# Kernel tuning notes

Measured on AMD Instinct MI355X. Metric: run time of the kernel, lower is better.

Reference implementation:

```python
import jax, jax.numpy as jnp
import numpy as np

IN_FEATURES = 4096
OUT_FEATURES = 4096
MAX_RANK = 32
ALPHA = 32
SCALING = ALPHA / MAX_RANK  # 1.0


def setup_inputs() -> dict:
    key = jax.random.key(0)
    k_x, k_u, k_v = jax.random.split(key, 3)
    x = jax.random.normal(k_x, (4, 2048, IN_FEATURES), dtype=jnp.float32)
    U = jax.random.normal(k_u, (OUT_FEATURES, MAX_RANK), dtype=jnp.float32) * 0.01
    S = jnp.ones((MAX_RANK,), dtype=jnp.float32)
    V = jax.random.normal(k_v, (MAX_RANK, IN_FEATURES), dtype=jnp.float32) * 0.01
    return {"x": x, "U": U, "S": S, "V": V}


def reference(x, U, S, V):
    # Original: W = U @ diag(S) @ V ; out = (x @ W.T) * scaling  (dropout=0 -> Identity)
    # Mathematically identical factored form: ((x @ V^T) * S) @ U^T * scaling.
    h = jnp.einsum('bsi,ri->bsr', x, V)        # [B,S,rank]
    h = h * S                                   # scale by singular values
    out = jnp.einsum('bsr,or->bso', h, U)       # [B,S,out]
    return out * SCALING
```

## Files before the change

### kernel.cpp

```cpp
#include <hip/hip_runtime.h>
#include <hip/hip_bf16.h>

typedef __bf16 bf16x8 __attribute__((ext_vector_type(8)));
typedef float  f32x4  __attribute__((ext_vector_type(4)));

#define IN_F   4096
#define OUT_F  4096
#define RANK   32

__device__ __forceinline__ bf16x8 cvt8(float4 a, float4 b) {
    bf16x8 r;
    r[0] = (__bf16)a.x; r[1] = (__bf16)a.y; r[2] = (__bf16)a.z; r[3] = (__bf16)a.w;
    r[4] = (__bf16)b.x; r[5] = (__bf16)b.y; r[6] = (__bf16)b.z; r[7] = (__bf16)b.w;
    return r;
}

template <int NSL>
__global__ __launch_bounds__(256, 3)
void lora_h(const float* __restrict__ X, const float* __restrict__ S,
            const float* __restrict__ V, float* __restrict__ Hpart)
{
    constexpr int SL    = IN_F / NSL;
    constexpr int STEPS = SL / 32;

    __shared__ float Hp[4][64][33];

    const int tid  = threadIdx.x;
    const int wave = tid >> 6;
    const int lane = tid & 63;
    const int r    = lane & 15;
    const int kg   = lane >> 4;

    const int t0 = blockIdx.x * 64;
    const int f0 = (blockIdx.y * 4 + wave) * SL;

    f32x4 acc[4][2] = {};

    const float* xb0 = X + (size_t)(t0 + r) * IN_F + f0 + kg * 8;
    const float* vb0 = V + (size_t)r * IN_F + f0 + kg * 8;

    #pragma unroll 2
    for (int s = 0; s < STEPS; ++s) {
        const float* xc = xb0 + s * 32;
        const float* vc = vb0 + s * 32;
        float4 v00 = *(const float4*)(vc);
        float4 v01 = *(const float4*)(vc + 4);
        float4 v10 = *(const float4*)(vc + (size_t)16 * IN_F);
        float4 v11 = *(const float4*)(vc + (size_t)16 * IN_F + 4);
        float4 x[4][2];
        #pragma unroll
        for (int tt = 0; tt < 4; ++tt) {
            x[tt][0] = *(const float4*)(xc + (size_t)tt * 16 * IN_F);
            x[tt][1] = *(const float4*)(xc + (size_t)tt * 16 * IN_F + 4);
        }
        bf16x8 vbf0 = cvt8(v00, v01);
        bf16x8 vbf1 = cvt8(v10, v11);
        #pragma unroll
        for (int tt = 0; tt < 4; ++tt) {
            bf16x8 xb = cvt8(x[tt][0], x[tt][1]);
            acc[tt][0] = __builtin_amdgcn_mfma_f32_16x16x32_bf16(xb, vbf0, acc[tt][0], 0, 0, 0);
            acc[tt][1] = __builtin_amdgcn_mfma_f32_16x16x32_bf16(xb, vbf1, acc[tt][1], 0, 0, 0);
        }
    }

    #pragma unroll
    for (int tt = 0; tt < 4; ++tt)
        #pragma unroll
        for (int rh = 0; rh < 2; ++rh)
            #pragma unroll
            for (int j = 0; j < 4; ++j)
                Hp[wave][tt * 16 + kg * 4 + j][rh * 16 + r] = acc[tt][rh][j];
    __syncthreads();

    float* dst = Hpart + (size_t)blockIdx.y * (8192 * RANK) + (size_t)t0 * RANK;
    for (int i = tid; i < 64 * RANK; i += 256) {
        const int tok = i >> 5, rk = i & 31;
        const float sum = Hp[0][tok][rk] + Hp[1][tok][rk]
                        + Hp[2][tok][rk] + Hp[3][tok][rk];
        dst[i] = sum * S[rk];
    }
}

template <int NKS>
__global__ __launch_bounds__(256)
void lora_hred(const float* __restrict__ Hpart, float* __restrict__ H)
{
    const int idx = blockIdx.x * 256 + threadIdx.x;
    const float4* hp = reinterpret_cast<const float4*>(Hpart);
    float4 v = hp[idx];
    #pragma unroll
    for (int k = 1; k < NKS; ++k) {
        float4 p = hp[(size_t)k * 65536 + idx];
        v.x += p.x; v.y += p.y; v.z += p.z; v.w += p.w;
    }
    reinterpret_cast<float4*>(H)[idx] = v;
}

__global__ __launch_bounds__(256, 4)
void lora_out(const float* __restrict__ H, const float* __restrict__ U,
              float* __restrict__ Out)
{
    __shared__ float Hs[32][33];

    const int tid  = threadIdx.x;
    const int wave = tid >> 6;
    const int lane = tid & 63;
    const int r    = lane & 15;
    const int kg   = lane >> 4;

    const int tt = blockIdx.x >> 2;
    const int cq = blockIdx.x & 3;
    const int t0 = tt * 32;

    {
        float4 v = reinterpret_cast<const float4*>(H + (size_t)t0 * RANK)[tid];
        const int tok = tid >> 3;
        const int rr  = (tid & 7) * 4;
        Hs[tok][rr] = v.x; Hs[tok][rr + 1] = v.y;
        Hs[tok][rr + 2] = v.z; Hs[tok][rr + 3] = v.w;
    }
    __syncthreads();

    bf16x8 hb[2];
    #pragma unroll
    for (int a = 0; a < 2; ++a)
        #pragma unroll
        for (int j = 0; j < 8; ++j) hb[a][j] = (__bf16)Hs[a * 16 + r][kg * 8 + j];

    const int wc0 = cq * 1024 + wave * 256;

    #pragma unroll
    for (int g = 0; g < 4; ++g) {
        float4 u0[4], u1[4];
        #pragma unroll
        for (int b = 0; b < 4; ++b) {
            const float4* up = reinterpret_cast<const float4*>(
                U + (size_t)(wc0 + g * 64 + b * 16 + r) * RANK + kg * 8);
            u0[b] = up[0];
            u1[b] = up[1];
        }
        #pragma unroll
        for (int b = 0; b < 4; ++b) {
            bf16x8 ub = cvt8(u0[b], u1[b]);
            #pragma unroll
            for (int a = 0; a < 2; ++a) {
                f32x4 d = {0.f, 0.f, 0.f, 0.f};
                d = __builtin_amdgcn_mfma_f32_16x16x32_bf16(ub, hb[a], d, 0, 0, 0);
                *reinterpret_cast<float4*>(
                    Out + (size_t)(t0 + a * 16 + r) * OUT_F
                        + wc0 + g * 64 + b * 16 + kg * 4)
                    = *reinterpret_cast<float4*>(&d);
            }
        }
    }
}

extern "C" void kernel_launch(void* const* d_in, const int* in_sizes, int n_in,
                              void* d_out, int out_size, void* d_ws, size_t ws_size,
                              hipStream_t stream) {
    const float* X = (const float*)d_in[0];
    const float* U = (const float*)d_in[1];
    const float* S = (const float*)d_in[2];
    const float* V = (const float*)d_in[3];
    float* Out = (float*)d_out;

    float* H     = (float*)d_ws;
    float* Hpart = (float*)d_ws + 262144;

    if (ws_size >= (size_t)10 * 1024 * 1024) {
        lora_h<32><<<dim3(128, 8), 256, 0, stream>>>(X, S, V, Hpart);
        lora_hred<8><<<256, 256, 0, stream>>>(Hpart, H);
        lora_out<<<1024, 256, 0, stream>>>(H, U, Out);
    } else if (ws_size >= (size_t)6 * 1024 * 1024) {
        lora_h<16><<<dim3(128, 4), 256, 0, stream>>>(X, S, V, Hpart);
        lora_hred<4><<<256, 256, 0, stream>>>(Hpart, H);
        lora_out<<<1024, 256, 0, stream>>>(H, U, Out);
    } else {
        lora_h<4><<<dim3(128, 1), 256, 0, stream>>>(X, S, V, H);
        lora_out<<<1024, 256, 0, stream>>>(H, U, Out);
    }
}
```

Baseline: 69.11 us.

## Retile LoRA down-projection to 16-token blocks with 4-way K split

The first-stage kernel now gives each block 16 tokens instead of 64 and splits the 4096 input features four ways instead of eight. Each wave handles a fixed 256-feature slice, using two MFMA accumulators and a fully unrolled 8-step loop. This makes 2048 small blocks with higher occupancy in place of 1024 larger ones, and it halves the partial-sum traffic in the reduction kernel. In exchange, each V load is now reused across only 16 tokens rather than 64, and a naive fallback replaces the small-workspace path.

Measured after the change: 88.57 us. 28.1% more time.

```diff
diff --git a/kernel.cpp b/kernel.cpp
--- a/kernel.cpp
+++ b/kernel.cpp
@@ -15,15 +15,11 @@
     return r;
 }
 
-template <int NSL>
-__global__ __launch_bounds__(256, 3)
+__global__ __launch_bounds__(256, 8)
 void lora_h(const float* __restrict__ X, const float* __restrict__ S,
             const float* __restrict__ V, float* __restrict__ Hpart)
 {
-    constexpr int SL    = IN_F / NSL;
-    constexpr int STEPS = SL / 32;
-
-    __shared__ float Hp[4][64][33];
+    __shared__ float Hp[4][16][33];
 
     const int tid  = threadIdx.x;
     const int wave = tid >> 6;
@@ -31,54 +27,56 @@
     const int r    = lane & 15;
     const int kg   = lane >> 4;
 
-    const int t0 = blockIdx.x * 64;
-    const int f0 = (blockIdx.y * 4 + wave) * SL;
+    const int t0 = blockIdx.x * 16;
+    const int f0 = blockIdx.y * 1024 + wave * 256 + kg * 8;
 
-    f32x4 acc[4][2] = {};
+    const float* xrow  = X + (size_t)(t0 + r) * IN_F + f0;
+    const float* v0row = V + (size_t)r        * IN_F + f0;
+    const float* v1row = V + (size_t)(16 + r) * IN_F + f0;
 
-    const float* xb0 = X + (size_t)(t0 + r) * IN_F + f0 + kg * 8;
-    const float* vb0 = V + (size_t)r * IN_F + f0 + kg * 8;
+    f32x4 a0 = {0.f, 0.f, 0.f, 0.f};
+    f32x4 a1 = {0.f, 0.f, 0.f, 0.f};
 
-    #pragma unroll 2
-    for (int s = 0; s < STEPS; ++s) {
-        const float* xc = xb0 + s * 32;
-        const float* vc = vb0 + s * 32;
-        float4 v00 = *(const float4*)(vc);
-        float4 v01 = *(const float4*)(vc + 4);
-        float4 v10 = *(const float4*)(vc + (size_t)16 * IN_F);
-        float4 v11 = *(const float4*)(vc + (size_t)16 * IN_F + 4);
-        float4 x[4][2];
-        #pragma unroll
-        for (int tt = 0; tt < 4; ++tt) {
-            x[tt][0] = *(const float4*)(xc + (size_t)tt * 16 * IN_F);
-            x[tt][1] = *(const float4*)(xc + (size_t)tt * 16 * IN_F + 4);
-        }
-        bf16x8 vbf0 = cvt8(v00, v01);
-        bf16x8 vbf1 = cvt8(v10, v11);
-        #pragma unroll
-        for (int tt = 0; tt < 4; ++tt) {
-            bf16x8 xb = cvt8(x[tt][0], x[tt][1]);
-            acc[tt][0] = __builtin_amdgcn_mfma_f32_16x16x32_bf16(xb, vbf0, acc[tt][0], 0, 0, 0);
-            acc[tt][1] = __builtin_amdgcn_mfma_f32_16x16x32_bf16(xb, vbf1, acc[tt][1], 0, 0, 0);
-        }
+    #pragma unroll
+    for (int s = 0; s < 8; ++s) {
+        const float4* xp  = reinterpret_cast<const float4*>(xrow  + s * 32);
+        const float4* vp0 = reinterpret_cast<const float4*>(v0row + s * 32);
+        const float4* vp1 = reinterpret_cast<const float4*>(v1row + s * 32);
+        float4 x0 = xp[0],  x1 = xp[1];
+        float4 va = vp0[0], vb = vp0[1];
+        float4 vc = vp1[0], vd = vp1[1];
+        bf16x8 xb = cvt8(x0, x1);
+        a0 = __builtin_amdgcn_mfma_f32_16x16x32_bf16(xb, cvt8(va, vb), a0, 0, 0, 0);
+        a1 = __builtin_amdgcn_mfma_f32_16x16x32_bf16(xb, cvt8(vc, vd), a1, 0, 0, 0);
     }
 
     #pragma unroll
-    for (int tt = 0; tt < 4; ++tt)
-        #pragma unroll
-        for (int rh = 0; rh < 2; ++rh)
-            #pragma unroll
-            for (int j = 0; j < 4; ++j)
-                Hp[wave][tt * 16 + kg * 4 + j][rh * 16 + r] = acc[tt][rh][j];
+    for (int j = 0; j < 4; ++j) {
+        Hp[wave][kg * 4 + j][r]      = a0[j];
+        Hp[wave][kg * 4 + j][16 + r] = a1[j];
+    }
     __syncthreads();
 
     float* dst = Hpart + (size_t)blockIdx.y * (8192 * RANK) + (size_t)t0 * RANK;
-    for (int i = tid; i < 64 * RANK; i += 256) {
+    #pragma unroll
+    for (int i = tid; i < 16 * RANK; i += 256) {
         const int tok = i >> 5, rk = i & 31;
         const float sum = Hp[0][tok][rk] + Hp[1][tok][rk]
                         + Hp[2][tok][rk] + Hp[3][tok][rk];
         dst[i] = sum * S[rk];
     }
+}
+
+__global__ __launch_bounds__(256)
+void lora_h_naive(const float* __restrict__ X, const float* __restrict__ S,
+                  const float* __restrict__ V, float* __restrict__ H)
+{
+    const int idx = blockIdx.x * 256 + threadIdx.x;
+    const int tok = idx >> 5, rk = idx & 31;
+    float acc = 0.f;
+    for (int f = 0; f < IN_F; ++f)
+        acc += X[(size_t)tok * IN_F + f] * V[(size_t)rk * IN_F + f];
+    H[idx] = acc * S[rk];
 }
 
 template <int NKS>
@@ -167,16 +165,12 @@
     float* H     = (float*)d_ws;
     float* Hpart = (float*)d_ws + 262144;
 
-    if (ws_size >= (size_t)10 * 1024 * 1024) {
-        lora_h<32><<<dim3(128, 8), 256, 0, stream>>>(X, S, V, Hpart);
-        lora_hred<8><<<256, 256, 0, stream>>>(Hpart, H);
-        lora_out<<<1024, 256, 0, stream>>>(H, U, Out);
-    } else if (ws_size >= (size_t)6 * 1024 * 1024) {
-        lora_h<16><<<dim3(128, 4), 256, 0, stream>>>(X, S, V, Hpart);
+    if (ws_size >= (size_t)5 * 1024 * 1024) {
+        lora_h<<<dim3(512, 4), 256, 0, stream>>>(X, S, V, Hpart);
         lora_hred<4><<<256, 256, 0, stream>>>(Hpart, H);
         lora_out<<<1024, 256, 0, stream>>>(H, U, Out);
     } else {
-        lora_h<4><<<dim3(128, 1), 256, 0, stream>>>(X, S, V, H);
+        lora_h_naive<<<1024, 256, 0, stream>>>(X, S, V, H);
         lora_out<<<1024, 256, 0, stream>>>(H, U, Out);
     }
 }
```
